# Optimization experiments

Measured on AMD Instinct MI355X. Metric: run time of the kernel, lower is better.

The kernel has to match this reference:

```python
import jax, jax.numpy as jnp
import numpy as np

N_GRAPHS = 1024  # number of disjoint graphs for global_mean_pool


def gcn_conv(x, src, dst, W, b, n):
    h = x @ W  # [N, out]
    deg = jax.ops.segment_sum(jnp.ones_like(dst, dtype=h.dtype), dst, num_segments=n) + 1.0  # +1 self loop
    dinv = jax.lax.rsqrt(deg)  # [N]
    coef = dinv[src] * dinv[dst]  # [E]
    agg = jax.ops.segment_sum(h[src] * coef[:, None], dst, num_segments=n)
    agg = agg + h * (dinv * dinv)[:, None]  # self-loop contribution
    return agg + b


def setup_inputs() -> dict:
    key = jax.random.key(0)
    ks = jax.random.split(key, 9)
    N, E, F_IN, H, D = 50000, 800000, 128, 256, 768
    x = jax.random.normal(ks[0], (N, F_IN), dtype=jnp.float32)
    edge_index = jax.random.randint(ks[1], (2, E), 0, N)
    batch = jnp.sort(jax.random.randint(ks[2], (N,), 0, N_GRAPHS))
    s = lambda k, sh, fan: jax.random.normal(k, sh, jnp.float32) * (1.0 / np.sqrt(fan))
    return dict(
        x=x, edge_index=edge_index, batch=batch,
        W1=s(ks[3], (F_IN, H), F_IN), b1=jnp.zeros((H,), jnp.float32),
        W2=s(ks[4], (H, H), H), b2=jnp.zeros((H,), jnp.float32),
        W3=s(ks[5], (H, H), H), b3=jnp.zeros((H,), jnp.float32),
        P1=s(ks[6], (H, H), H), pb1=jnp.zeros((H,), jnp.float32),
        P2=s(ks[7], (H, D), H), pb2=jnp.zeros((D,), jnp.float32),
        ln_g=jnp.ones((D,), jnp.float32), ln_b=jnp.zeros((D,), jnp.float32),
    )


def reference(x, edge_index, batch, W1, b1, W2, b2, W3, b3, P1, pb1, P2, pb2, ln_g, ln_b):
    n = x.shape[0]
    src, dst = edge_index[0], edge_index[1]
    h1 = jax.nn.relu(gcn_conv(x, src, dst, W1, b1, n))
    h2 = jax.nn.relu(gcn_conv(h1, src, dst, W2, b2, n)) + h1
    h3 = jax.nn.relu(gcn_conv(h2, src, dst, W3, b3, n)) + h2
    # global_mean_pool
    sums = jax.ops.segment_sum(h3, batch, num_segments=N_GRAPHS)
    cnt = jax.ops.segment_sum(jnp.ones((n,), h3.dtype), batch, num_segments=N_GRAPHS)
    g = sums / jnp.maximum(cnt, 1.0)[:, None]  # [G, 256]
    # projection MLP (dropout is identity in eval)
    g = jax.nn.relu(g @ P1 + pb1) @ P2 + pb2  # [G, D]
    # LayerNorm
    mu = jnp.mean(g, axis=-1, keepdims=True)
    var = jnp.mean((g - mu) ** 2, axis=-1, keepdims=True)
    return (g - mu) * jax.lax.rsqrt(var + 1e-5) * ln_g + ln_b
```

## Files before the change

kernel.cpp:

```cpp
#include <hip/hip_runtime.h>


typedef __attribute__((ext_vector_type(8))) short short8;
typedef __attribute__((ext_vector_type(4))) float f32x4;
typedef __attribute__((ext_vector_type(2))) float f32x2;

__device__ __forceinline__ float bf2f(unsigned short s) {
    union { unsigned u; float f; } v;
    v.u = ((unsigned)s) << 16;
    return v.f;
}
__device__ __forceinline__ unsigned short f2bf(float f) {
    union { float f; unsigned u; } v;
    v.f = f;
    unsigned r = (v.u + 0x7FFFu + ((v.u >> 16) & 1u)) >> 16;
    return (unsigned short)r;
}

__device__ __forceinline__ void acc8_fp8(unsigned int lo, unsigned int hi, float* acc) {
    f32x2 p0 = __builtin_amdgcn_cvt_pk_f32_fp8(lo, false);
    f32x2 p1 = __builtin_amdgcn_cvt_pk_f32_fp8(lo, true);
    f32x2 p2 = __builtin_amdgcn_cvt_pk_f32_fp8(hi, false);
    f32x2 p3 = __builtin_amdgcn_cvt_pk_f32_fp8(hi, true);
    acc[0] += p0[0]; acc[1] += p0[1]; acc[2] += p1[0]; acc[3] += p1[1];
    acc[4] += p2[0]; acc[5] += p2[1]; acc[6] += p3[0]; acc[7] += p3[1];
}


__global__ void count_kernel(const int* __restrict__ dst, int E, int* __restrict__ cnt,
                             int* __restrict__ rank) {
    int e = blockIdx.x * blockDim.x + threadIdx.x;
    if (e < E) rank[e] = atomicAdd(&cnt[dst[e]], 1);
}

__global__ void scanA(const int* __restrict__ cnt, int n, int* __restrict__ bsum,
                      float* __restrict__ dinv) {
    int tid = threadIdx.x, lane = tid & 63, w = tid >> 6;
    int i = blockIdx.x * 512 + tid;
    int v = (i < n) ? cnt[i] : 0;
    if (i < n) dinv[i] = rsqrtf((float)v + 1.0f);
    int s = v;
    #pragma unroll
    for (int off = 1; off < 64; off <<= 1) s += __shfl_xor(s, off);
    __shared__ int ws[8];
    if (lane == 0) ws[w] = s;
    __syncthreads();
    if (tid == 0) {
        int t = 0;
        #pragma unroll
        for (int j = 0; j < 8; j++) t += ws[j];
        bsum[blockIdx.x] = t;
    }
}

__global__ void scanC(const int* __restrict__ cnt, int n, const int* __restrict__ bsum,
                      int E, int* __restrict__ row_ptr) {
    int tid = threadIdx.x, lane = tid & 63, w = tid >> 6;
    int i = blockIdx.x * 512 + tid;
    __shared__ int s_boff;
    if (tid < 64) {
        int acc = 0;
        for (int b = tid; b < blockIdx.x; b += 64) acc += bsum[b];
        #pragma unroll
        for (int off = 1; off < 64; off <<= 1) acc += __shfl_xor(acc, off);
        if (tid == 0) s_boff = acc;
    }
    int v = (i < n) ? cnt[i] : 0;
    int incl = v;
    #pragma unroll
    for (int off = 1; off < 64; off <<= 1) {
        int t = __shfl_up(incl, off);
        if (lane >= off) incl += t;
    }
    __shared__ int ws[8];
    if (lane == 63) ws[w] = incl;
    __syncthreads();
    int woff = 0;
    for (int j = 0; j < w; j++) woff += ws[j];
    if (i < n) row_ptr[i] = s_boff + woff + incl - v;
    if (blockIdx.x == 0 && tid == 0) row_ptr[n] = E;
}


__global__ void convert_all(const int* __restrict__ src, const int* __restrict__ dst,
                            const int* __restrict__ row_ptr, const int* __restrict__ rank,
                            int* __restrict__ csr, int E,
                            const float* __restrict__ x, const float* __restrict__ dinv,
                            unsigned char* __restrict__ xf8, int n4,
                            const float* __restrict__ W1, const float* __restrict__ W2,
                            const float* __restrict__ W3, const float* __restrict__ P1,
                            const float* __restrict__ P2,
                            unsigned short* __restrict__ Wt1, unsigned short* __restrict__ Wt2,
                            unsigned short* __restrict__ Wt3, unsigned short* __restrict__ Pt1,
                            unsigned short* __restrict__ Pt2,
                            int F_IN, int H, int D,
                            unsigned char* __restrict__ zx,
                            unsigned char* __restrict__ z1,
                            unsigned char* __restrict__ z2) {
    int gidx = blockIdx.x * blockDim.x + threadIdx.x;
    if (gidx < E) {
        csr[row_ptr[dst[gidx]] + rank[gidx]] = src[gidx];
        return;
    }
    int idx = gidx - E;
    if (idx < n4) {
        float di = dinv[idx >> 5];
        float4 v = ((const float4*)x)[idx];
        unsigned int p = 0;
        p = __builtin_amdgcn_cvt_pk_fp8_f32(di * v.x, di * v.y, p, false);
        p = __builtin_amdgcn_cvt_pk_fp8_f32(di * v.z, di * v.w, p, true);
        ((unsigned int*)xf8)[idx] = p;
        return;
    }
    int t = idx - n4;
    int n1 = F_IN * H, n2 = H * H, n5 = H * D;
    const float* W; unsigned short* O; int N;
    if (t < n1)              { W = W1; O = Wt1; N = H; }
    else if ((t -= n1) < n2) { W = W2; O = Wt2; N = H; }
    else if ((t -= n2) < n2) { W = W3; O = Wt3; N = H; }
    else if ((t -= n2) < n2) { W = P1; O = Pt1; N = H; }
    else if ((t -= n2) < n5) { W = P2; O = Pt2; N = D; }
    else {
        t -= n5;
        if (t < 128) zx[t] = 0;
        else if (t < 384) z1[t - 128] = 0;
        else if (t < 640) z2[t - 384] = 0;
        return;
    }
    int k = t / N, n = t - k * N;
    int K = (W == W1) ? F_IN : H;
    O[(size_t)n * K + k] = f2bf(W[t]);
}


__launch_bounds__(256)
__global__ void aggregate256(const unsigned char* __restrict__ hf8,
                             const int* __restrict__ row_ptr,
                             const int* __restrict__ csr,
                             unsigned short* __restrict__ out, int n, int zrow) {
    int node = blockIdx.x * 4 + (threadIdx.x >> 6);
    int lane = threadIdx.x & 63;
    if (node >= n) return;
    int half = lane >> 5;
    int cl = lane & 31;
    float acc[8] = {0, 0, 0, 0, 0, 0, 0, 0};
    if (half == 0) {
        uint2 sv = *(const uint2*)(hf8 + (size_t)node * 256 + cl * 8);
        acc8_fp8(sv.x, sv.y, acc);
    }
    int beg = row_ptr[node], end = row_ptr[node + 1];
    for (int base = beg; base < end; base += 64) {
        int k = base + lane;
        int mi = (k < end) ? csr[k] : zrow;
        int cnt = min(64, end - base);
        for (int j = 0; j < cnt; j += 16) {
            int idx[8]; uint2 vv[8];
            #pragma unroll
            for (int u = 0; u < 8; u++) idx[u] = __shfl(mi, j + 2 * u + half);
            #pragma unroll
            for (int u = 0; u < 8; u++) vv[u] = *(const uint2*)(hf8 + (size_t)idx[u] * 256 + cl * 8);
            #pragma unroll
            for (int u = 0; u < 8; u++) acc8_fp8(vv[u].x, vv[u].y, acc);
        }
    }
    #pragma unroll
    for (int c = 0; c < 8; c++) acc[c] += __shfl_xor(acc[c], 32);
    if (half == 0) {
        short8 o;
        #pragma unroll
        for (int c = 0; c < 8; c++) o[c] = (short)f2bf(acc[c]);
        *(short8*)(out + (size_t)node * 256 + cl * 8) = o;
    }
}

__launch_bounds__(256)
__global__ void aggregate128(const unsigned char* __restrict__ hf8,
                             const int* __restrict__ row_ptr,
                             const int* __restrict__ csr,
                             unsigned short* __restrict__ out, int n, int zrow) {
    int node = blockIdx.x * 4 + (threadIdx.x >> 6);
    int lane = threadIdx.x & 63;
    if (node >= n) return;
    int qtr = lane >> 4;
    int cl = lane & 15;
    float acc[8] = {0, 0, 0, 0, 0, 0, 0, 0};
    if (qtr == 0) {
        uint2 sv = *(const uint2*)(hf8 + (size_t)node * 128 + cl * 8);
        acc8_fp8(sv.x, sv.y, acc);
    }
    int beg = row_ptr[node], end = row_ptr[node + 1];
    for (int base = beg; base < end; base += 64) {
        int k = base + lane;
        int mi = (k < end) ? csr[k] : zrow;
        int cnt = min(64, end - base);
        for (int j = 0; j < cnt; j += 32) {
            int idx[8]; uint2 vv[8];
            #pragma unroll
            for (int u = 0; u < 8; u++) idx[u] = __shfl(mi, j + 4 * u + qtr);
            #pragma unroll
            for (int u = 0; u < 8; u++) vv[u] = *(const uint2*)(hf8 + (size_t)idx[u] * 128 + cl * 8);
            #pragma unroll
            for (int u = 0; u < 8; u++) acc8_fp8(vv[u].x, vv[u].y, acc);
        }
    }
    #pragma unroll
    for (int c = 0; c < 8; c++) {
        acc[c] += __shfl_xor(acc[c], 16);
        acc[c] += __shfl_xor(acc[c], 32);
    }
    if (qtr == 0) {
        short8 o;
        #pragma unroll
        for (int c = 0; c < 8; c++) o[c] = (short)f2bf(acc[c]);
        *(short8*)(out + (size_t)node * 128 + cl * 8) = o;
    }
}


template<int K, int RELU, int RES, int OUTF32, int SCALE, int FP8O>
__launch_bounds__(256)
__global__ void wgemm(const unsigned short* __restrict__ A,
                      const unsigned short* __restrict__ Bt,
                      const float* __restrict__ bias,
                      const unsigned short* __restrict__ residual,
                      const float* __restrict__ dinv,
                      void* __restrict__ Cout,
                      unsigned char* __restrict__ f8out,
                      int M, int N, int ntiles) {
    constexpr int KK = K / 32;
    constexpr int S = K + 8;
    constexpr int CS = 65;
    constexpr int BSZ = 64 * S * 2;
    constexpr int CSZ = 128 * CS * 4;
    constexpr int SM = BSZ > CSZ ? BSZ : CSZ;
    __shared__ __align__(16) char smraw[SM];
    unsigned short* Bs = (unsigned short*)smraw;
    float* Cs = (float*)smraw;
    constexpr int CPR = K / 8;

    int tid = threadIdx.x;
    int wave = tid >> 6, lane = tid & 63;
    int r = lane & 15, q = lane >> 4;
    int mr = blockIdx.y * 128 + wave * 32;
    int nbase = blockIdx.x * ntiles * 64;

    short8 a[2][KK];
    #pragma unroll
    for (int mi = 0; mi < 2; mi++) {
        int arow = mr + mi * 16 + r;
        bool ok = arow < M;
        const unsigned short* ap = A + (size_t)(ok ? arow : 0) * K;
        #pragma unroll
        for (int kk = 0; kk < KK; kk++) {
            short8 v = *(const short8*)(ap + kk * 32 + q * 8);
            if (!ok) v = (short8){0, 0, 0, 0, 0, 0, 0, 0};
            a[mi][kk] = v;
        }
    }

    for (int t = 0; t < ntiles; t++) {
        int n0 = nbase + t * 64;
        if (t > 0) __syncthreads();
        #pragma unroll
        for (int pass = 0; pass < 64 * CPR / 256; pass++) {
            int f = pass * 256 + tid;
            int row = f / CPR, ch = f % CPR;
            *(short8*)&Bs[row * S + ch * 8] =
                *(const short8*)(Bt + (size_t)(n0 + row) * K + ch * 8);
        }
        __syncthreads();

        f32x4 acc[2][4];
        #pragma unroll
        for (int mi = 0; mi < 2; mi++)
            #pragma unroll
            for (int j = 0; j < 4; j++) acc[mi][j] = (f32x4){0.f, 0.f, 0.f, 0.f};

        #pragma unroll
        for (int kk = 0; kk < KK; kk++) {
            short8 b[4];
            #pragma unroll
            for (int j = 0; j < 4; j++)
                b[j] = *(short8*)&Bs[(j * 16 + r) * S + kk * 32 + q * 8];
            #pragma unroll
            for (int mi = 0; mi < 2; mi++)
                #pragma unroll
                for (int j = 0; j < 4; j++)
                    acc[mi][j] = __builtin_amdgcn_mfma_f32_16x16x32_bf16(a[mi][kk], b[j], acc[mi][j], 0, 0, 0);
        }

        __syncthreads();
        #pragma unroll
        for (int mi = 0; mi < 2; mi++)
            #pragma unroll
            for (int j = 0; j < 4; j++)
                #pragma unroll
                for (int p = 0; p < 4; p++)
                    Cs[(wave * 32 + mi * 16 + q * 4 + p) * CS + j * 16 + r] = acc[mi][j][p];
        __syncthreads();

        int row = tid >> 1;
        int halfc = (tid & 1) * 32;
        int grow = blockIdx.y * 128 + row;
        if (grow < M) {
            float vals[32];
            #pragma unroll
            for (int c = 0; c < 8; c++)
                *(f32x4*)&vals[c * 4] = *(f32x4*)&Cs[row * CS + halfc + c * 4];
            float di = 1.f, rdi = 1.f;
            if (SCALE) { di = dinv[grow]; if (RES) rdi = 1.f / di; }
            float bb[32];
            #pragma unroll
            for (int c = 0; c < 8; c++)
                *(f32x4*)&bb[c * 4] = *(const f32x4*)&bias[n0 + halfc + c * 4];
            short8 rv[4];
            if (RES) {
                #pragma unroll
                for (int c = 0; c < 4; c++)
                    rv[c] = *(const short8*)(residual + (size_t)grow * N + n0 + halfc + c * 8);
            }
            #pragma unroll
            for (int c = 0; c < 32; c++) {
                float v = (SCALE ? di * vals[c] : vals[c]) + bb[c];
                if (RELU) v = fmaxf(v, 0.f);
                if (RES) v += bf2f((unsigned short)rv[c / 8][c % 8]) * rdi;
                if (SCALE == 1) v *= di;
                vals[c] = v;
            }
            if (OUTF32) {
                float* cp = (float*)Cout + (size_t)grow * N + n0 + halfc;
                #pragma unroll
                for (int c = 0; c < 8; c++) *(f32x4*)&cp[c * 4] = *(f32x4*)&vals[c * 4];
            } else {
                unsigned short* cp = (unsigned short*)Cout + (size_t)grow * N + n0 + halfc;
                #pragma unroll
                for (int c = 0; c < 4; c++) {
                    short8 o;
                    #pragma unroll
                    for (int u = 0; u < 8; u++) o[u] = (short)f2bf(vals[c * 8 + u]);
                    *(short8*)&cp[c * 8] = o;
                }
            }
            if (FP8O) {
                unsigned int w[8];
                #pragma unroll
                for (int c = 0; c < 8; c++) {
                    unsigned int p = 0;
                    p = __builtin_amdgcn_cvt_pk_fp8_f32(vals[c * 4 + 0], vals[c * 4 + 1], p, false);
                    p = __builtin_amdgcn_cvt_pk_fp8_f32(vals[c * 4 + 2], vals[c * 4 + 3], p, true);
                    w[c] = p;
                }
                unsigned char* fp = f8out + (size_t)grow * N + n0 + halfc;
                *(uint4*)(fp) = make_uint4(w[0], w[1], w[2], w[3]);
                *(uint4*)(fp + 16) = make_uint4(w[4], w[5], w[6], w[7]);
            }
        }
    }
}


__launch_bounds__(256)
__global__ void pool_kernel(const unsigned short* __restrict__ h, const int* __restrict__ batch,
                            unsigned short* __restrict__ g0, int n, int G) {
    int g = blockIdx.x * 4 + (threadIdx.x >> 6);
    int lane = threadIdx.x & 63;
    if (g >= G) return;
    int lo = 0, hi = 0;
    if (lane == 0) {
        int a = 0, b = n;
        while (a < b) { int m = (a + b) >> 1; if (batch[m] < g) a = m + 1; else b = m; }
        lo = a;
        int a2 = a, b2 = n;
        while (a2 < b2) { int m = (a2 + b2) >> 1; if (batch[m] < g + 1) a2 = m + 1; else b2 = m; }
        hi = a2;
    }
    lo = __shfl(lo, 0); hi = __shfl(hi, 0);
    float a0 = 0.f, a1 = 0.f, a2 = 0.f, a3 = 0.f;
    for (int i = lo; i < hi; i++) {
        ushort4 v = *(const ushort4*)(h + (size_t)i * 256 + lane * 4);
        a0 += bf2f(v.x); a1 += bf2f(v.y); a2 += bf2f(v.z); a3 += bf2f(v.w);
    }
    float inv = 1.0f / fmaxf((float)(hi - lo), 1.0f);
    ushort4 o;
    o.x = f2bf(a0 * inv); o.y = f2bf(a1 * inv); o.z = f2bf(a2 * inv); o.w = f2bf(a3 * inv);
    *(ushort4*)(g0 + (size_t)g * 256 + lane * 4) = o;
}

__launch_bounds__(256)
__global__ void ln_kernel(const float* __restrict__ g2, const float* __restrict__ gamma,
                          const float* __restrict__ beta, float* __restrict__ out, int rows) {
    int row = blockIdx.x * 4 + (threadIdx.x >> 6);
    int lane = threadIdx.x & 63;
    if (row >= rows) return;
    const float* r = g2 + (size_t)row * 768;
    float v[12];
    float s = 0.f, s2 = 0.f;
    #pragma unroll
    for (int j = 0; j < 12; j++) {
        v[j] = r[lane + 64 * j];
        s += v[j];
        s2 += v[j] * v[j];
    }
    #pragma unroll
    for (int off = 32; off > 0; off >>= 1) {
        s += __shfl_down(s, off);
        s2 += __shfl_down(s2, off);
    }
    s = __shfl(s, 0);
    s2 = __shfl(s2, 0);
    float mu = s * (1.0f / 768.0f);
    float var = s2 * (1.0f / 768.0f) - mu * mu;
    float inv = rsqrtf(var + 1e-5f);
    #pragma unroll
    for (int j = 0; j < 12; j++) {
        int c = lane + 64 * j;
        out[(size_t)row * 768 + c] = (v[j] - mu) * inv * gamma[c] + beta[c];
    }
}


extern "C" void kernel_launch(void* const* d_in, const int* in_sizes, int n_in,
                              void* d_out, int out_size, void* d_ws, size_t ws_size,
                              hipStream_t stream) {
    const float* x    = (const float*)d_in[0];
    const int* eidx   = (const int*)d_in[1];
    const int* batch  = (const int*)d_in[2];
    const float* W1   = (const float*)d_in[3];
    const float* b1   = (const float*)d_in[4];
    const float* W2   = (const float*)d_in[5];
    const float* b2   = (const float*)d_in[6];
    const float* W3   = (const float*)d_in[7];
    const float* b3   = (const float*)d_in[8];
    const float* P1   = (const float*)d_in[9];
    const float* pb1  = (const float*)d_in[10];
    const float* P2   = (const float*)d_in[11];
    const float* pb2  = (const float*)d_in[12];
    const float* ln_g = (const float*)d_in[13];
    const float* ln_b = (const float*)d_in[14];
    float* out = (float*)d_out;

    const int N = in_sizes[2];
    const int E = in_sizes[1] / 2;
    const int F_IN = in_sizes[0] / N;
    const int H = in_sizes[4];
    const int D = in_sizes[12];
    const int G = out_size / D;
    const int NPAD = (N + 127) & ~127;
    const int NB = (N + 511) / 512;

    const int* src = eidx;
    const int* dst = eidx + E;

    char* ws = (char*)d_ws;
    size_t off = 0;
    auto alloc = [&](size_t bytes) -> char* {
        char* p = ws + off;
        off = (off + bytes + 255) & ~(size_t)255;
        return p;
    };
    int*   cnt      = (int*)alloc((size_t)NPAD * 4);
    float* dinv     = (float*)alloc((size_t)NPAD * 4);
    int*   row_ptr  = (int*)alloc((size_t)(N + 1) * 4);
    int*   bsum     = (int*)alloc(128 * 4);
    int*   rank     = (int*)alloc((size_t)E * 4);
    int*   csr      = (int*)alloc((size_t)E * 4);
    unsigned char* xf8  = (unsigned char*)alloc((size_t)(N + 1) * F_IN);
    unsigned char* h1f8 = (unsigned char*)alloc((size_t)(N + 1) * H);
    unsigned char* h2f8 = (unsigned char*)alloc((size_t)(N + 1) * H);
    unsigned short* Wt1 = (unsigned short*)alloc((size_t)F_IN * H * 2);
    unsigned short* Wt2 = (unsigned short*)alloc((size_t)H * H * 2);
    unsigned short* Wt3 = (unsigned short*)alloc((size_t)H * H * 2);
    unsigned short* Pt1 = (unsigned short*)alloc((size_t)H * H * 2);
    unsigned short* Pt2 = (unsigned short*)alloc((size_t)H * D * 2);
    unsigned short* t1  = (unsigned short*)alloc((size_t)N * F_IN * 2);
    unsigned short* tA  = (unsigned short*)alloc((size_t)N * H * 2);
    unsigned short* hh1 = (unsigned short*)alloc((size_t)N * H * 2);
    unsigned short* hh2 = (unsigned short*)alloc((size_t)N * H * 2);
    unsigned short* h3  = (unsigned short*)alloc((size_t)N * H * 2);
    unsigned short* g0b = (unsigned short*)alloc((size_t)G * H * 2);
    unsigned short* g1b = (unsigned short*)alloc((size_t)G * H * 2);
    float* g2 = (float*)alloc((size_t)G * D * 4);
    (void)ws_size; (void)n_in;

    hipMemsetAsync(cnt, 0, (size_t)NPAD * 4, stream);
    count_kernel<<<(E + 255) / 256, 256, 0, stream>>>(dst, E, cnt, rank);
    scanA<<<NB, 512, 0, stream>>>(cnt, N, bsum, dinv);
    scanC<<<NB, 512, 0, stream>>>(cnt, N, bsum, E, row_ptr);

    {
        int n4 = N * F_IN / 4;
        int tot = F_IN * H + 3 * H * H + H * D;
        int total = E + n4 + tot + 640;
        convert_all<<<(total + 255) / 256, 256, 0, stream>>>(
            src, dst, row_ptr, rank, csr, E,
            x, dinv, xf8, n4, W1, W2, W3, P1, P2, Wt1, Wt2, Wt3, Pt1, Pt2, F_IN, H, D,
            xf8 + (size_t)N * F_IN, h1f8 + (size_t)N * H, h2f8 + (size_t)N * H);
    }

    int agg_grid = (N + 3) / 4;
    int mtiles = (N + 127) / 128;

    aggregate128<<<agg_grid, 256, 0, stream>>>(xf8, row_ptr, csr, t1, N, N);
    wgemm<128, 1, 0, 0, 1, 1><<<dim3(4, mtiles), 256, 0, stream>>>(t1, Wt1, b1, nullptr, dinv, hh1, h1f8, N, H, 1);

    aggregate256<<<agg_grid, 256, 0, stream>>>(h1f8, row_ptr, csr, tA, N, N);
    wgemm<256, 1, 1, 0, 1, 1><<<dim3(4, mtiles), 256, 0, stream>>>(tA, Wt2, b2, hh1, dinv, hh2, h2f8, N, H, 1);

    aggregate256<<<agg_grid, 256, 0, stream>>>(h2f8, row_ptr, csr, tA, N, N);
    wgemm<256, 1, 1, 0, 2, 0><<<dim3(4, mtiles), 256, 0, stream>>>(tA, Wt3, b3, hh2, dinv, h3, nullptr, N, H, 1);

    pool_kernel<<<(G + 3) / 4, 256, 0, stream>>>(h3, batch, g0b, N, G);
    wgemm<256, 1, 0, 0, 0, 0><<<dim3(4, G / 128), 256, 0, stream>>>(g0b, Pt1, pb1, nullptr, nullptr, g1b, nullptr, G, H, 1);
    wgemm<256, 0, 0, 1, 0, 0><<<dim3(12, G / 128), 256, 0, stream>>>(g1b, Pt2, pb2, nullptr, nullptr, g2, nullptr, G, D, 1);
    ln_kernel<<<G / 4, 256, 0, stream>>>(g2, ln_g, ln_b, out, G);
}
```

Measured before the change: 372.1 us.

## Replace LDS-staged GEMM epilogue with register transpose via cross-lane shuffles

```diff
diff --git a/kernel.cpp b/kernel.cpp
--- a/kernel.cpp
+++ b/kernel.cpp
@@ -15,6 +15,12 @@
     v.f = f;
     unsigned r = (v.u + 0x7FFFu + ((v.u >> 16) & 1u)) >> 16;
     return (unsigned short)r;
+}
+__device__ __forceinline__ unsigned pk2bf(float lo, float hi) {
+    return (unsigned)f2bf(lo) | ((unsigned)f2bf(hi) << 16);
+}
+__device__ __forceinline__ unsigned short u4c(ushort4 v, int p) {
+    return p == 0 ? v.x : p == 1 ? v.y : p == 2 ? v.z : v.w;
 }
 
 __device__ __forceinline__ void acc8_fp8(unsigned int lo, unsigned int hi, float* acc) {
@@ -229,14 +235,8 @@
                       int M, int N, int ntiles) {
     constexpr int KK = K / 32;
     constexpr int S = K + 8;
-    constexpr int CS = 65;
-    constexpr int BSZ = 64 * S * 2;
-    constexpr int CSZ = 128 * CS * 4;
-    constexpr int SM = BSZ > CSZ ? BSZ : CSZ;
-    __shared__ __align__(16) char smraw[SM];
-    unsigned short* Bs = (unsigned short*)smraw;
-    float* Cs = (float*)smraw;
     constexpr int CPR = K / 8;
+    __shared__ __align__(16) unsigned short Bs[64 * S];
 
     int tid = threadIdx.x;
     int wave = tid >> 6, lane = tid & 63;
@@ -248,12 +248,12 @@
     #pragma unroll
     for (int mi = 0; mi < 2; mi++) {
         int arow = mr + mi * 16 + r;
-        bool ok = arow < M;
-        const unsigned short* ap = A + (size_t)(ok ? arow : 0) * K;
+        bool aok = arow < M;
+        const unsigned short* ap = A + (size_t)(aok ? arow : 0) * K;
         #pragma unroll
         for (int kk = 0; kk < KK; kk++) {
             short8 v = *(const short8*)(ap + kk * 32 + q * 8);
-            if (!ok) v = (short8){0, 0, 0, 0, 0, 0, 0, 0};
+            if (!aok) v = (short8){0, 0, 0, 0, 0, 0, 0, 0};
             a[mi][kk] = v;
         }
     }
@@ -286,73 +286,121 @@
             for (int mi = 0; mi < 2; mi++)
                 #pragma unroll
                 for (int j = 0; j < 4; j++)
-                    acc[mi][j] = __builtin_amdgcn_mfma_f32_16x16x32_bf16(a[mi][kk], b[j], acc[mi][j], 0, 0, 0);
+                    acc[mi][j] = __builtin_amdgcn_mfma_f32_16x16x32_bf16(b[j], a[mi][kk], acc[mi][j], 0, 0, 0);
         }
 
-        __syncthreads();
-        #pragma unroll
-        for (int mi = 0; mi < 2; mi++)
+        f32x4 bq[4];
+        #pragma unroll
+        for (int j = 0; j < 4; j++)
+            bq[j] = *(const f32x4*)&bias[n0 + j * 16 + q * 4];
+
+        #pragma unroll
+        for (int mi = 0; mi < 2; mi++) {
+            int m = mr + mi * 16 + r;
+            bool ok = m < M;
+            float di = 1.f, rdi = 1.f;
+            if (SCALE) { di = dinv[ok ? m : 0]; if (RES) rdi = 1.f / di; }
+            ushort4 rv[4];
+            if (RES) {
+                const unsigned short* rp = residual + (size_t)(ok ? m : 0) * N + n0 + q * 4;
+                #pragma unroll
+                for (int j = 0; j < 4; j++) rv[j] = *(const ushort4*)(rp + j * 16);
+            }
+            float u[4][4];
             #pragma unroll
             for (int j = 0; j < 4; j++)
                 #pragma unroll
-                for (int p = 0; p < 4; p++)
-                    Cs[(wave * 32 + mi * 16 + q * 4 + p) * CS + j * 16 + r] = acc[mi][j][p];
-        __syncthreads();
-
-        int row = tid >> 1;
-        int halfc = (tid & 1) * 32;
-        int grow = blockIdx.y * 128 + row;
-        if (grow < M) {
-            float vals[32];
-            #pragma unroll
-            for (int c = 0; c < 8; c++)
-                *(f32x4*)&vals[c * 4] = *(f32x4*)&Cs[row * CS + halfc + c * 4];
-            float di = 1.f, rdi = 1.f;
-            if (SCALE) { di = dinv[grow]; if (RES) rdi = 1.f / di; }
-            float bb[32];
-            #pragma unroll
-            for (int c = 0; c < 8; c++)
-                *(f32x4*)&bb[c * 4] = *(const f32x4*)&bias[n0 + halfc + c * 4];
-            short8 rv[4];
-            if (RES) {
-                #pragma unroll
-                for (int c = 0; c < 4; c++)
-                    rv[c] = *(const short8*)(residual + (size_t)grow * N + n0 + halfc + c * 8);
-            }
-            #pragma unroll
-            for (int c = 0; c < 32; c++) {
-                float v = (SCALE ? di * vals[c] : vals[c]) + bb[c];
-                if (RELU) v = fmaxf(v, 0.f);
-                if (RES) v += bf2f((unsigned short)rv[c / 8][c % 8]) * rdi;
-                if (SCALE == 1) v *= di;
-                vals[c] = v;
-            }
+                for (int p = 0; p < 4; p++) {
+                    float v = (SCALE ? di * acc[mi][j][p] : acc[mi][j][p]) + bq[j][p];
+                    if (RELU) v = fmaxf(v, 0.f);
+                    if (RES) v += bf2f(u4c(rv[j], p)) * rdi;
+                    if (SCALE == 1) v *= di;
+                    u[j][p] = v;
+                }
+
             if (OUTF32) {
-                float* cp = (float*)Cout + (size_t)grow * N + n0 + halfc;
-                #pragma unroll
-                for (int c = 0; c < 8; c++) *(f32x4*)&cp[c * 4] = *(f32x4*)&vals[c * 4];
+                float c4[4][4], tf[4][4];
+                #pragma unroll
+                for (int j = 0; j < 4; j++)
+                    #pragma unroll
+                    for (int d = 0; d < 4; d++) c4[j][d] = u[j][d];
+                #pragma unroll
+                for (int j = 0; j < 4; j++)
+                    #pragma unroll
+                    for (int d = 0; d < 4; d++) tf[j][d] = __shfl_xor(c4[j ^ 1][d], 16);
+                #pragma unroll
+                for (int j = 0; j < 4; j++)
+                    #pragma unroll
+                    for (int d = 0; d < 4; d++)
+                        c4[j][d] = (((j ^ q) & 1) == 0) ? c4[j][d] : tf[j][d];
+                #pragma unroll
+                for (int j = 0; j < 4; j++)
+                    #pragma unroll
+                    for (int d = 0; d < 4; d++) tf[j][d] = __shfl_xor(c4[j ^ 2][d], 32);
+                #pragma unroll
+                for (int j = 0; j < 4; j++)
+                    #pragma unroll
+                    for (int d = 0; d < 4; d++)
+                        c4[j][d] = (((j ^ q) & 2) == 0) ? c4[j][d] : tf[j][d];
+                if (ok) {
+                    float* cp = (float*)Cout + (size_t)m * N + n0 + q * 16;
+                    #pragma unroll
+                    for (int j = 0; j < 4; j++) *(f32x4*)&cp[j * 4] = *(f32x4*)&c4[j][0];
+                }
             } else {
-                unsigned short* cp = (unsigned short*)Cout + (size_t)grow * N + n0 + halfc;
-                #pragma unroll
-                for (int c = 0; c < 4; c++) {
-                    short8 o;
-                    #pragma unroll
-                    for (int u = 0; u < 8; u++) o[u] = (short)f2bf(vals[c * 8 + u]);
-                    *(short8*)&cp[c * 8] = o;
+                unsigned db[4][2], tb[4][2];
+                #pragma unroll
+                for (int j = 0; j < 4; j++) {
+                    db[j][0] = pk2bf(u[j][0], u[j][1]);
+                    db[j][1] = pk2bf(u[j][2], u[j][3]);
                 }
-            }
-            if (FP8O) {
-                unsigned int w[8];
-                #pragma unroll
-                for (int c = 0; c < 8; c++) {
-                    unsigned int p = 0;
-                    p = __builtin_amdgcn_cvt_pk_fp8_f32(vals[c * 4 + 0], vals[c * 4 + 1], p, false);
-                    p = __builtin_amdgcn_cvt_pk_fp8_f32(vals[c * 4 + 2], vals[c * 4 + 3], p, true);
-                    w[c] = p;
+                #pragma unroll
+                for (int j = 0; j < 4; j++)
+                    #pragma unroll
+                    for (int d = 0; d < 2; d++) tb[j][d] = __shfl_xor((int)db[j ^ 1][d], 16);
+                #pragma unroll
+                for (int j = 0; j < 4; j++)
+                    #pragma unroll
+                    for (int d = 0; d < 2; d++)
+                        db[j][d] = (((j ^ q) & 1) == 0) ? db[j][d] : tb[j][d];
+                #pragma unroll
+                for (int j = 0; j < 4; j++)
+                    #pragma unroll
+                    for (int d = 0; d < 2; d++) tb[j][d] = __shfl_xor((int)db[j ^ 2][d], 32);
+                #pragma unroll
+                for (int j = 0; j < 4; j++)
+                    #pragma unroll
+                    for (int d = 0; d < 2; d++)
+                        db[j][d] = (((j ^ q) & 2) == 0) ? db[j][d] : tb[j][d];
+                if (ok) {
+                    unsigned short* cp = (unsigned short*)Cout + (size_t)m * N + n0 + q * 16;
+                    *(uint4*)cp = make_uint4(db[0][0], db[0][1], db[1][0], db[1][1]);
+                    *(uint4*)(cp + 8) = make_uint4(db[2][0], db[2][1], db[3][0], db[3][1]);
                 }
-                unsigned char* fp = f8out + (size_t)grow * N + n0 + halfc;
-                *(uint4*)(fp) = make_uint4(w[0], w[1], w[2], w[3]);
-                *(uint4*)(fp + 16) = make_uint4(w[4], w[5], w[6], w[7]);
+                if (FP8O) {
+                    unsigned f8[4], t8[4];
+                    #pragma unroll
+                    for (int j = 0; j < 4; j++) {
+                        unsigned p8 = 0;
+                        p8 = __builtin_amdgcn_cvt_pk_fp8_f32(u[j][0], u[j][1], p8, false);
+                        p8 = __builtin_amdgcn_cvt_pk_fp8_f32(u[j][2], u[j][3], p8, true);
+                        f8[j] = p8;
+                    }
+                    #pragma unroll
+                    for (int j = 0; j < 4; j++) t8[j] = __shfl_xor((int)f8[j ^ 1], 16);
+                    #pragma unroll
+                    for (int j = 0; j < 4; j++)
+                        f8[j] = (((j ^ q) & 1) == 0) ? f8[j] : t8[j];
+                    #pragma unroll
+                    for (int j = 0; j < 4; j++) t8[j] = __shfl_xor((int)f8[j ^ 2], 32);
+                    #pragma unroll
+                    for (int j = 0; j < 4; j++)
+                        f8[j] = (((j ^ q) & 2) == 0) ? f8[j] : t8[j];
+                    if (ok) {
+                        unsigned char* fp = f8out + (size_t)m * N + n0 + q * 16;
+                        *(uint4*)fp = make_uint4(f8[0], f8[1], f8[2], f8[3]);
+                    }
+                }
             }
         }
     }
```

New measurement: 370.8 us. No clear change (-0.4%).
